# Kernel optimization log

Measured on AMD Instinct MI355X. Metric: run time of the kernel, lower is better.

The kernel has to match this reference:

```python
import jax, jax.numpy as jnp
import numpy as np
from jax.ops import segment_sum

N = 50000
E = 1600000
B = 1000  # number of graphs
F_IN, H, OUT = 64, 128, 10


def setup_inputs() -> dict:
    key = jax.random.key(0)
    ks = jax.random.split(key, 16)
    x = jax.random.normal(ks[0], (N, F_IN), dtype=jnp.float32)
    edge_index = jax.random.randint(ks[1], (2, E), 0, N, dtype=jnp.int64)
    batch = jnp.sort(jax.random.randint(ks[2], (N,), 0, B, dtype=jnp.int64))

    def glorot(k, fan_in, fan_out):
        s = jnp.sqrt(6.0 / (fan_in + fan_out))
        return jax.random.uniform(k, (fan_in, fan_out), jnp.float32, -s, s)

    return {
        "x": x, "edge_index": edge_index, "batch": batch,
        "W1": glorot(ks[3], F_IN, H), "b1": jnp.zeros((H,), jnp.float32),
        "W2": glorot(ks[4], H, H), "b2": jnp.zeros((H,), jnp.float32),
        "W3": glorot(ks[5], H, H // 2), "b3": jnp.zeros((H // 2,), jnp.float32),
        "Wl1": glorot(ks[6], H // 2, H // 4), "bl1": jnp.zeros((H // 4,), jnp.float32),
        "Wl2": glorot(ks[7], H // 4, OUT), "bl2": jnp.zeros((OUT,), jnp.float32),
    }


def _gcn_conv(x, src, dst, dinv, W, b):
    # GCNConv: h = x W; out_i = sum_{j->i} dinv_j * dinv_i * h_j ; + bias
    h = x @ W
    norm = dinv[src] * dinv[dst]                      # [E+N]
    msg = h[src] * norm[:, None]                      # gather + scale
    out = segment_sum(msg, dst, num_segments=N)       # scatter-add
    return out + b


def reference(x, edge_index, batch, W1, b1, W2, b2, W3, b3, Wl1, bl1, Wl2, bl2):
    # add self-loops (static shape E+N)
    loops = jnp.arange(N, dtype=edge_index.dtype)
    src = jnp.concatenate([edge_index[0], loops])
    dst = jnp.concatenate([edge_index[1], loops])
    # symmetric degree normalization from target degrees (incl. self-loops)
    deg = segment_sum(jnp.ones_like(dst, dtype=x.dtype), dst, num_segments=N)
    dinv = jnp.where(deg > 0, jax.lax.rsqrt(jnp.maximum(deg, 1.0)), 0.0)

    h = jax.nn.relu(_gcn_conv(x, src, dst, dinv, W1, b1))   # dropout: eval mode (identity)
    h = jax.nn.relu(_gcn_conv(h, src, dst, dinv, W2, b2))
    h = jax.nn.relu(_gcn_conv(h, src, dst, dinv, W3, b3))

    # global mean pool over graphs
    sums = segment_sum(h, batch, num_segments=B)            # [B, H//2]
    cnts = segment_sum(jnp.ones((N,), h.dtype), batch, num_segments=B)
    g = sums / jnp.maximum(cnts, 1.0)[:, None]

    g = jax.nn.relu(g @ Wl1 + bl1)
    return g @ Wl2 + bl2
```

## Files before the change

kernel.cpp:

```cpp
#include <hip/hip_runtime.h>
#include <hip/hip_bf16.h>
#include <hip/hip_fp16.h>

#define CHUNK 8192
#define WN    128
#define NBMAX 512

typedef _Float16 f16x8 __attribute__((ext_vector_type(8)));
typedef float    f32x4 __attribute__((ext_vector_type(4)));


__global__ __launch_bounds__(1024) void k_rhist(const int* __restrict__ dst, int* __restrict__ H,
                                                int E, int NC, int NB) {
    __shared__ int h[NBMAX];
    int c = blockIdx.x, t = threadIdx.x;
    for (int i = t; i < NB; i += 1024) h[i] = 0;
    __syncthreads();
    int base = c * CHUNK;
    int lim = min(CHUNK, E - base);
    for (int k = t; k < lim; k += 1024) atomicAdd(&h[dst[base + k] >> 7], 1);
    __syncthreads();
    for (int i = t; i < NB; i += 1024) H[i * NC + c] = h[i];
}

__global__ __launch_bounds__(256) void k_scanA(const int* __restrict__ in, int* __restrict__ out,
                                               int* __restrict__ bsum, int n) {
    __shared__ int s[256];
    int i = blockIdx.x * 256 + threadIdx.x;
    int v = (i < n) ? in[i] : 0;
    s[threadIdx.x] = v;
    __syncthreads();
    for (int off = 1; off < 256; off <<= 1) {
        int x = (threadIdx.x >= off) ? s[threadIdx.x - off] : 0;
        __syncthreads();
        s[threadIdx.x] += x;
        __syncthreads();
    }
    if (i < n) out[i] = s[threadIdx.x] - v;
    if (threadIdx.x == 255) bsum[blockIdx.x] = s[255];
}

__global__ __launch_bounds__(512) void k_scanB(int* __restrict__ bsum, int nb) {
    __shared__ int s[512];
    int t = threadIdx.x;
    int v = (t < nb) ? bsum[t] : 0;
    s[t] = v;
    __syncthreads();
    for (int off = 1; off < 512; off <<= 1) {
        int x = (t >= off) ? s[t - off] : 0;
        __syncthreads();
        s[t] += x;
        __syncthreads();
    }
    if (t < nb) bsum[t] = s[t] - v;
}

__global__ __launch_bounds__(256) void k_scanC(int* __restrict__ out, const int* __restrict__ bsum,
                                               int n) {
    int i = blockIdx.x * 256 + threadIdx.x;
    if (i < n) out[i] += bsum[blockIdx.x];
}

__global__ __launch_bounds__(1024) void k_rscatter(const int* __restrict__ src, const int* __restrict__ dst,
                                                   const int* __restrict__ O, int* __restrict__ packed,
                                                   int E, int NC, int NB) {
    __shared__ int cur[NBMAX];
    int c = blockIdx.x, t = threadIdx.x;
    for (int i = t; i < NB; i += 1024) cur[i] = O[i * NC + c];
    __syncthreads();
    int base = c * CHUNK;
    int lim = min(CHUNK, E - base);
    for (int k = t; k < lim; k += 1024) {
        int d = dst[base + k];
        int p = atomicAdd(&cur[d >> 7], 1);
        packed[p] = (src[base + k] << 7) | (d & (WN - 1));
    }
}

__global__ __launch_bounds__(512) void k_wincsr(const int* __restrict__ packed,
                                                const int* __restrict__ O,
                                                int* __restrict__ row_start,
                                                int* __restrict__ csr,
                                                float* __restrict__ dinv,
                                                const float* __restrict__ x,
                                                __half* __restrict__ y,
                                                int n, int NC, int NB, int E) {
    __shared__ int cnt[WN];
    __shared__ int ss[WN];
    __shared__ int cur[WN];
    __shared__ float sdv[WN];
    int b = blockIdx.x, t = threadIdx.x;
    int s = O[b * NC];
    int e = (b + 1 < NB) ? O[(b + 1) * NC] : E;
    if (t < WN) cnt[t] = 0;
    __syncthreads();
    for (int k = s + t; k < e; k += 512) atomicAdd(&cnt[packed[k] & (WN - 1)], 1);
    __syncthreads();
    int v = (t < WN) ? cnt[t] : 0;
    if (t < WN) ss[t] = v;
    __syncthreads();
    for (int off = 1; off < WN; off <<= 1) {
        int x2 = (t >= off && t < WN) ? ss[t - off] : 0;
        __syncthreads();
        if (t < WN) ss[t] += x2;
        __syncthreads();
    }
    int node = b * WN + t;
    if (t < WN) {
        int start = s + ss[t] - v;
        cur[t] = start;
        float dv = rsqrtf((float)(cnt[t] + 1));
        sdv[t] = dv;
        if (node < n) {
            row_start[node] = start;
            dinv[node] = dv;
        }
    }
    if (b == NB - 1 && t == 0) row_start[n] = E;
    __syncthreads();
    for (int k = s + t; k < e; k += 512) {
        int r = packed[k];
        int p = atomicAdd(&cur[r & (WN - 1)], 1);
        csr[p] = r >> 7;
    }
    int node0 = b * WN;
    for (int i = t; i < WN * 16; i += 512) {
        int nd = i >> 4, c4 = i & 15;
        int g = node0 + nd;
        if (g < n) {
            float dv = sdv[nd];
            float4 vv = ((const float4*)x)[(size_t)g * 16 + c4];
            __half2 h0 = __floats2half2_rn(vv.x * dv, vv.y * dv);
            __half2 h1 = __floats2half2_rn(vv.z * dv, vv.w * dv);
            uint2 u;
            u.x = *(unsigned int*)&h0;
            u.y = *(unsigned int*)&h1;
            ((uint2*)y)[(size_t)g * 16 + c4] = u;
        }
    }
}


__global__ __launch_bounds__(256) void k_w2h3(const float* __restrict__ W1, _Float16* __restrict__ W1t,
                                              const float* __restrict__ W2, _Float16* __restrict__ W2t,
                                              const float* __restrict__ W3, _Float16* __restrict__ W3t) {
    int idx = blockIdx.x * 256 + threadIdx.x;
    if (idx < 8192) {
        int k = idx >> 7, f = idx & 127;
        W1t[f * 64 + k] = (_Float16)W1[idx];
    } else if (idx < 24576) {
        int i = idx - 8192;
        int k = i >> 7, f = i & 127;
        W2t[f * 128 + k] = (_Float16)W2[i];
    } else if (idx < 32768) {
        int i = idx - 24576;
        int k = i >> 6, f = i & 63;
        W3t[f * 128 + k] = (_Float16)W3[i];
    }
}


template <int K, int F, int EPI, bool SP>
__global__ __launch_bounds__(256) void k_gemm_mfma(const __half* __restrict__ X,
                                                   const _Float16* __restrict__ Wt,
                                                   const float* __restrict__ dinv,
                                                   const float* __restrict__ bias,
                                                   __half* __restrict__ Hl,
                                                   __half* __restrict__ Hh, int n) {
    constexpr int ROWS = 64;
    constexpr int XS   = K + 8;
    __shared__ _Float16 sX[ROWS * XS];
    __shared__ _Float16 sW[F * XS];
    int row0 = blockIdx.x * ROWS;
    int t = threadIdx.x;

    const uint4* Xg = (const uint4*)X;
    for (int i = t; i < ROWS * (K / 8); i += 256) {
        int r = i / (K / 8), k8 = i % (K / 8);
        int gr = row0 + r;
        uint4 v = (gr < n) ? Xg[(size_t)gr * (K / 8) + k8] : make_uint4(0, 0, 0, 0);
        *(uint4*)&sX[r * XS + k8 * 8] = v;
    }
    const uint4* Wg = (const uint4*)Wt;
    for (int i = t; i < F * (K / 8); i += 256) {
        int f = i / (K / 8), k8 = i % (K / 8);
        *(uint4*)&sW[f * XS + k8 * 8] = Wg[i];
    }
    __syncthreads();

    int w = t >> 6, l = t & 63;
    int wrow = w * 16;
    int lr = l & 15;
    int lk = (l >> 4) * 8;
    f32x4 acc[F / 16];
#pragma unroll
    for (int c = 0; c < F / 16; ++c) acc[c] = (f32x4){0.f, 0.f, 0.f, 0.f};

#pragma unroll
    for (int kb = 0; kb < K / 32; ++kb) {
        f16x8 a = *(const f16x8*)&sX[(wrow + lr) * XS + kb * 32 + lk];
#pragma unroll
        for (int c = 0; c < F / 16; ++c) {
            f16x8 b = *(const f16x8*)&sW[(c * 16 + lr) * XS + kb * 32 + lk];
            acc[c] = __builtin_amdgcn_mfma_f32_16x16x32_f16(a, b, acc[c], 0, 0, 0);
        }
    }

    int rbase = row0 + wrow + (l >> 4) * 4;
    if (EPI == 0) {
        float dv[4];
#pragma unroll
        for (int r = 0; r < 4; ++r) dv[r] = (rbase + r < n) ? dinv[rbase + r] : 0.f;
#pragma unroll
        for (int c = 0; c < F / 16; ++c) {
            int col = c * 16 + lr;
#pragma unroll
            for (int r = 0; r < 4; ++r) {
                int gr = rbase + r;
                if (gr < n) {
                    __half hv = __float2half(acc[c][r] * dv[r]);
                    if (SP) {
                        if (c < F / 32) Hl[(size_t)gr * (F / 2) + col] = hv;
                        else            Hh[(size_t)gr * (F / 2) + col - F / 2] = hv;
                    } else {
                        Hl[(size_t)gr * F + col] = hv;
                    }
                }
            }
        }
    } else {
#pragma unroll
        for (int c = 0; c < F / 16; ++c) {
            int col = c * 16 + lr;
            float bc = bias[col];
#pragma unroll
            for (int r = 0; r < 4; ++r) {
                int gr = rbase + r;
                if (gr < n) {
                    __half hv = __float2half(fmaxf(acc[c][r] + bc, 0.f));
                    if (SP) {
                        if (c < F / 32) Hl[(size_t)gr * (F / 2) + col] = hv;
                        else            Hh[(size_t)gr * (F / 2) + col - F / 2] = hv;
                    } else {
                        Hl[(size_t)gr * F + col] = hv;
                    }
                }
            }
        }
    }
}


__device__ __forceinline__ void acc8(float* a, uint4 v) {
    const __half2* h = (const __half2*)&v;
#pragma unroll
    for (int i = 0; i < 4; ++i) {
        float2 f = __half22float2(h[i]);
        a[2 * i]     += f.x;
        a[2 * i + 1] += f.y;
    }
}

template <int F, int EPI>
__global__ void k_agg_h(const __half* __restrict__ HN, const int* __restrict__ csr,
                        const int* __restrict__ rs, const float* __restrict__ dinv,
                        const float* __restrict__ bias, __half* __restrict__ OUT,
                        int n, int ostride4, int ooff4) {
    constexpr int LPN = F / 8;
    constexpr int NPB = 256 / LPN;
    int node = blockIdx.x * NPB + threadIdx.x / LPN;
    int l    = threadIdx.x % LPN;
    if (node >= n) return;
    const uint4* hn = (const uint4*)HN;
    size_t base = (size_t)node * LPN + l;
    float a[8];
    {
        uint4 v = hn[base];
        const __half2* h = (const __half2*)&v;
#pragma unroll
        for (int i = 0; i < 4; ++i) {
            float2 f = __half22float2(h[i]);
            a[2 * i] = f.x; a[2 * i + 1] = f.y;
        }
    }
    int s = rs[node], e = rs[node + 1];
    int k = s;
    for (; k + 8 <= e; k += 8) {
        int si[8];
#pragma unroll
        for (int u = 0; u < 8; ++u) si[u] = csr[k + u];
        uint4 v[8];
#pragma unroll
        for (int u = 0; u < 8; ++u) v[u] = hn[(size_t)si[u] * LPN + l];
#pragma unroll
        for (int u = 0; u < 8; ++u) acc8(a, v[u]);
    }
    for (; k + 4 <= e; k += 4) {
        int s0 = csr[k], s1 = csr[k + 1], s2 = csr[k + 2], s3 = csr[k + 3];
        uint4 v0 = hn[(size_t)s0 * LPN + l];
        uint4 v1 = hn[(size_t)s1 * LPN + l];
        uint4 v2 = hn[(size_t)s2 * LPN + l];
        uint4 v3 = hn[(size_t)s3 * LPN + l];
        acc8(a, v0); acc8(a, v1); acc8(a, v2); acc8(a, v3);
    }
    for (; k < e; ++k) acc8(a, hn[(size_t)csr[k] * LPN + l]);

    float dv = dinv[node];
    float o[8];
    if (EPI == 0) {
#pragma unroll
        for (int j = 0; j < 8; ++j) o[j] = a[j] * dv;
    } else {
        const float4* b4 = (const float4*)bias;
        float4 bb0 = b4[l * 2], bb1 = b4[l * 2 + 1];
        o[0] = fmaxf(fmaf(a[0], dv, bb0.x), 0.f);
        o[1] = fmaxf(fmaf(a[1], dv, bb0.y), 0.f);
        o[2] = fmaxf(fmaf(a[2], dv, bb0.z), 0.f);
        o[3] = fmaxf(fmaf(a[3], dv, bb0.w), 0.f);
        o[4] = fmaxf(fmaf(a[4], dv, bb1.x), 0.f);
        o[5] = fmaxf(fmaf(a[5], dv, bb1.y), 0.f);
        o[6] = fmaxf(fmaf(a[6], dv, bb1.z), 0.f);
        o[7] = fmaxf(fmaf(a[7], dv, bb1.w), 0.f);
    }
    uint4 u;
    __half2 p0 = __floats2half2_rn(o[0], o[1]);
    __half2 p1 = __floats2half2_rn(o[2], o[3]);
    __half2 p2 = __floats2half2_rn(o[4], o[5]);
    __half2 p3 = __floats2half2_rn(o[6], o[7]);
    u.x = *(unsigned int*)&p0; u.y = *(unsigned int*)&p1;
    u.z = *(unsigned int*)&p2; u.w = *(unsigned int*)&p3;
    ((uint4*)OUT)[(size_t)node * ostride4 + ooff4 + l] = u;
}


__global__ void k_gstart(const int* __restrict__ batch, int* __restrict__ gstart,
                         int n, int B) {
    int i = blockIdx.x * 256 + threadIdx.x;
    if (i >= n) return;
    int b = batch[i];
    if (i == 0) {
        for (int g = 0; g <= b; ++g) gstart[g] = 0;
    } else {
        int prev = batch[i - 1];
        if (prev != b)
            for (int g = prev + 1; g <= b; ++g) gstart[g] = i;
    }
    if (i == n - 1)
        for (int g = b + 1; g <= B; ++g) gstart[g] = n;
}

__global__ void k_poolhead(const __half* __restrict__ H3, const int* __restrict__ gstart,
                           const float* __restrict__ Wl1, const float* __restrict__ bl1,
                           const float* __restrict__ Wl2, const float* __restrict__ bl2,
                           float* __restrict__ out, int B) {
    __shared__ float sh[4][64];
    __shared__ float shid[4][32];
    int w = threadIdx.x >> 6;
    int lane = threadIdx.x & 63;
    int g = blockIdx.x * 4 + w;
    if (g < B) {
        int s = gstart[g], e = gstart[g + 1];
        float acc = 0.f;
        for (int i = s; i < e; ++i) acc += __half2float(H3[(size_t)i * 64 + lane]);
        float cnt = fmaxf((float)(e - s), 1.f);
        sh[w][lane] = acc / cnt;
    }
    __syncthreads();
    if (g < B && lane < 32) {
        float a = bl1[lane];
        for (int k = 0; k < 64; ++k) a = fmaf(sh[w][k], Wl1[k * 32 + lane], a);
        shid[w][lane] = fmaxf(a, 0.f);
    }
    __syncthreads();
    if (g < B && lane < 10) {
        float a = bl2[lane];
        for (int k = 0; k < 32; ++k) a = fmaf(shid[w][k], Wl2[k * 10 + lane], a);
        out[g * 10 + lane] = a;
    }
}


extern "C" void kernel_launch(void* const* d_in, const int* in_sizes, int n_in,
                              void* d_out, int out_size, void* d_ws, size_t ws_size,
                              hipStream_t stream) {
    const float* x    = (const float*)d_in[0];
    const int*   ei   = (const int*)d_in[1];
    const int*   batch= (const int*)d_in[2];
    const float* W1   = (const float*)d_in[3];
    const float* b1   = (const float*)d_in[4];
    const float* W2   = (const float*)d_in[5];
    const float* b2   = (const float*)d_in[6];
    const float* W3   = (const float*)d_in[7];
    const float* b3   = (const float*)d_in[8];
    const float* Wl1  = (const float*)d_in[9];
    const float* bl1  = (const float*)d_in[10];
    const float* Wl2  = (const float*)d_in[11];
    const float* bl2  = (const float*)d_in[12];

    const int N  = in_sizes[0] / 64;
    const int E  = in_sizes[1] / 2;
    const int B  = out_size / 10;
    const int NB = (N + WN - 1) / WN;
    const int NC = (E + CHUNK - 1) / CHUNK;
    const int NBNC = NB * NC;
    const int GS = (NBNC + 255) / 256;
    const int* srcI = ei;
    const int* dstI = ei + E;

    char* p = (char*)d_ws;
    auto alloc = [&](size_t bytes) {
        char* r = p;
        p += (bytes + 255) & ~(size_t)255;
        return r;
    };
    int*   H        = (int*)alloc((size_t)NBNC * 4);
    int*   O        = (int*)alloc((size_t)NBNC * 4);
    int*   bsum     = (int*)alloc(2048 * 4);
    int*   packed   = (int*)alloc((size_t)E * 4);
    int*   csr      = (int*)alloc((size_t)E * 4);
    int*   row_start= (int*)alloc((size_t)(N + 1) * 4);
    float* dinv     = (float*)alloc((size_t)N * 4);
    int*   gstart   = (int*)alloc((size_t)(B + 1) * 4);
    _Float16* W1t   = (_Float16*)alloc((size_t)64 * 128 * 2);
    _Float16* W2t   = (_Float16*)alloc((size_t)128 * 128 * 2);
    _Float16* W3t   = (_Float16*)alloc((size_t)128 * 64 * 2);
    __half* bufA    = (__half*)alloc((size_t)N * 128 * 2);
    __half* bufB    = (__half*)alloc((size_t)N * 128 * 2);
    __half* bufB2   = bufB + (size_t)N * 64;

    int gN = (N + 255) / 256;
    int gG = (N + 63) / 64;

    k_rhist   <<<NC, 1024, 0, stream>>>(dstI, H, E, NC, NB);
    k_scanA   <<<GS, 256, 0, stream>>>(H, O, bsum, NBNC);
    k_scanB   <<<1, 512, 0, stream>>>(bsum, GS);
    k_scanC   <<<GS, 256, 0, stream>>>(O, bsum, NBNC);
    k_rscatter<<<NC, 1024, 0, stream>>>(srcI, dstI, O, packed, E, NC, NB);
    k_wincsr  <<<NB, 512, 0, stream>>>(packed, O, row_start, csr, dinv, x, bufA,
                                       N, NC, NB, E);

    k_w2h3<<<128, 256, 0, stream>>>(W1, W1t, W2, W2t, W3, W3t);

    k_agg_h<64, 0><<<(N + 31) / 32, 256, 0, stream>>>(bufA, csr, row_start, dinv,
                                                      dinv, bufB, N, 8, 0);
    k_gemm_mfma<64, 128, 1, false><<<gG, 256, 0, stream>>>(bufB, W1t, dinv, b1,
                                                           bufA, nullptr, N);
    k_gemm_mfma<128, 128, 0, true><<<gG, 256, 0, stream>>>(bufA, W2t, dinv, b2,
                                                           bufB, bufB2, N);
    k_agg_h<64, 1><<<(N + 31) / 32, 256, 0, stream>>>(bufB,  csr, row_start, dinv,
                                                      b2,      bufA, N, 16, 0);
    k_agg_h<64, 1><<<(N + 31) / 32, 256, 0, stream>>>(bufB2, csr, row_start, dinv,
                                                      b2 + 64, bufA, N, 16, 8);
    k_gemm_mfma<128, 64, 0, false><<<gG, 256, 0, stream>>>(bufA, W3t, dinv, b3,
                                                           bufB, nullptr, N);
    k_agg_h<64, 1><<<(N + 31) / 32, 256, 0, stream>>>(bufB, csr, row_start, dinv,
                                                      b3, bufB2, N, 8, 0);

    k_gstart  <<<gN, 256, 0, stream>>>(batch, gstart, N, B);
    k_poolhead<<<(B + 3) / 4, 256, 0, stream>>>(bufB2, gstart, Wl1, bl1, Wl2, bl2,
                                                (float*)d_out, B);
}
```

Baseline: 205.2 us.

## Fuse scan fixup, merge layer-2 aggregations, fold mean-pool into last aggregation

Drops the scanC kernel by adding the block prefix offsets directly where O is read in the scatter and window-CSR kernels. The two per-half aggregation launches of layer 2 become a single launch that uses a 2-D grid. The final aggregation no longer writes H3; it atomically adds each node's output into per-graph float sums and counts, which removes the gstart kernel and the serial per-graph sum loop in the pool head. In exchange there are many float atomics on 1000 graph rows, a memset of the accumulators, and a summation order that is no longer deterministic.

```diff
diff --git a/kernel.cpp b/kernel.cpp
--- a/kernel.cpp
+++ b/kernel.cpp
@@ -55,18 +55,16 @@
     if (t < nb) bsum[t] = s[t] - v;
 }
 
-__global__ __launch_bounds__(256) void k_scanC(int* __restrict__ out, const int* __restrict__ bsum,
-                                               int n) {
-    int i = blockIdx.x * 256 + threadIdx.x;
-    if (i < n) out[i] += bsum[blockIdx.x];
-}
 
 __global__ __launch_bounds__(1024) void k_rscatter(const int* __restrict__ src, const int* __restrict__ dst,
-                                                   const int* __restrict__ O, int* __restrict__ packed,
-                                                   int E, int NC, int NB) {
+                                                   const int* __restrict__ O, const int* __restrict__ bsum,
+                                                   int* __restrict__ packed, int E, int NC, int NB) {
     __shared__ int cur[NBMAX];
     int c = blockIdx.x, t = threadIdx.x;
-    for (int i = t; i < NB; i += 1024) cur[i] = O[i * NC + c];
+    for (int i = t; i < NB; i += 1024) {
+        int idx = i * NC + c;
+        cur[i] = O[idx] + bsum[idx >> 8];
+    }
     __syncthreads();
     int base = c * CHUNK;
     int lim = min(CHUNK, E - base);
@@ -79,6 +77,7 @@
 
 __global__ __launch_bounds__(512) void k_wincsr(const int* __restrict__ packed,
                                                 const int* __restrict__ O,
+                                                const int* __restrict__ bsum,
                                                 int* __restrict__ row_start,
                                                 int* __restrict__ csr,
                                                 float* __restrict__ dinv,
@@ -90,8 +89,15 @@
     __shared__ int cur[WN];
     __shared__ float sdv[WN];
     int b = blockIdx.x, t = threadIdx.x;
-    int s = O[b * NC];
-    int e = (b + 1 < NB) ? O[(b + 1) * NC] : E;
+    int i0 = b * NC;
+    int s = O[i0] + bsum[i0 >> 8];
+    int e;
+    if (b + 1 < NB) {
+        int i1 = (b + 1) * NC;
+        e = O[i1] + bsum[i1 >> 8];
+    } else {
+        e = E;
+    }
     if (t < WN) cnt[t] = 0;
     __syncthreads();
     for (int k = s + t; k < e; k += 512) atomicAdd(&cnt[packed[k] & (WN - 1)], 1);
@@ -261,13 +267,20 @@
     }
 }
 
-template <int F, int EPI>
-__global__ void k_agg_h(const __half* __restrict__ HN, const int* __restrict__ csr,
-                        const int* __restrict__ rs, const float* __restrict__ dinv,
-                        const float* __restrict__ bias, __half* __restrict__ OUT,
-                        int n, int ostride4, int ooff4) {
+template <int F, int EPI, int POOL>
+__global__ void k_agg_h(const __half* __restrict__ HN0, const __half* __restrict__ HN1,
+                        const int* __restrict__ csr, const int* __restrict__ rs,
+                        const float* __restrict__ dinv,
+                        const float* __restrict__ bias0, const float* __restrict__ bias1,
+                        __half* __restrict__ OUT, int n, int ostride4,
+                        const int* __restrict__ batch, float* __restrict__ gsum,
+                        int* __restrict__ gcnt) {
     constexpr int LPN = F / 8;
     constexpr int NPB = 256 / LPN;
+    int half = blockIdx.y;
+    const __half* HN = half ? HN1 : HN0;
+    const float* bias = half ? bias1 : bias0;
+    int ooff4 = half ? LPN : 0;
     int node = blockIdx.x * NPB + threadIdx.x / LPN;
     int l    = threadIdx.x % LPN;
     if (node >= n) return;
@@ -322,34 +335,26 @@
         o[6] = fmaxf(fmaf(a[6], dv, bb1.z), 0.f);
         o[7] = fmaxf(fmaf(a[7], dv, bb1.w), 0.f);
     }
-    uint4 u;
-    __half2 p0 = __floats2half2_rn(o[0], o[1]);
-    __half2 p1 = __floats2half2_rn(o[2], o[3]);
-    __half2 p2 = __floats2half2_rn(o[4], o[5]);
-    __half2 p3 = __floats2half2_rn(o[6], o[7]);
-    u.x = *(unsigned int*)&p0; u.y = *(unsigned int*)&p1;
-    u.z = *(unsigned int*)&p2; u.w = *(unsigned int*)&p3;
-    ((uint4*)OUT)[(size_t)node * ostride4 + ooff4 + l] = u;
-}
-
-
-__global__ void k_gstart(const int* __restrict__ batch, int* __restrict__ gstart,
-                         int n, int B) {
-    int i = blockIdx.x * 256 + threadIdx.x;
-    if (i >= n) return;
-    int b = batch[i];
-    if (i == 0) {
-        for (int g = 0; g <= b; ++g) gstart[g] = 0;
+    if (POOL) {
+        int bg = batch[node];
+        float* gs = &gsum[bg * 64 + l * 8];
+#pragma unroll
+        for (int j = 0; j < 8; ++j) atomicAdd(&gs[j], o[j]);
+        if (l == 0) atomicAdd(&gcnt[bg], 1);
     } else {
-        int prev = batch[i - 1];
-        if (prev != b)
-            for (int g = prev + 1; g <= b; ++g) gstart[g] = i;
-    }
-    if (i == n - 1)
-        for (int g = b + 1; g <= B; ++g) gstart[g] = n;
-}
-
-__global__ void k_poolhead(const __half* __restrict__ H3, const int* __restrict__ gstart,
+        uint4 u;
+        __half2 p0 = __floats2half2_rn(o[0], o[1]);
+        __half2 p1 = __floats2half2_rn(o[2], o[3]);
+        __half2 p2 = __floats2half2_rn(o[4], o[5]);
+        __half2 p3 = __floats2half2_rn(o[6], o[7]);
+        u.x = *(unsigned int*)&p0; u.y = *(unsigned int*)&p1;
+        u.z = *(unsigned int*)&p2; u.w = *(unsigned int*)&p3;
+        ((uint4*)OUT)[(size_t)node * ostride4 + ooff4 + l] = u;
+    }
+}
+
+
+__global__ void k_poolhead(const float* __restrict__ gsum, const int* __restrict__ gcnt,
                            const float* __restrict__ Wl1, const float* __restrict__ bl1,
                            const float* __restrict__ Wl2, const float* __restrict__ bl2,
                            float* __restrict__ out, int B) {
@@ -359,11 +364,8 @@
     int lane = threadIdx.x & 63;
     int g = blockIdx.x * 4 + w;
     if (g < B) {
-        int s = gstart[g], e = gstart[g + 1];
-        float acc = 0.f;
-        for (int i = s; i < e; ++i) acc += __half2float(H3[(size_t)i * 64 + lane]);
-        float cnt = fmaxf((float)(e - s), 1.f);
-        sh[w][lane] = acc / cnt;
+        float cnt = fmaxf((float)gcnt[g], 1.f);
+        sh[w][lane] = gsum[g * 64 + lane] / cnt;
     }
     __syncthreads();
     if (g < B && lane < 32) {
@@ -413,6 +415,9 @@
         p += (bytes + 255) & ~(size_t)255;
         return r;
     };
+    float* gsum     = (float*)alloc((size_t)B * 64 * 4);
+    int*   gcnt     = (int*)alloc((size_t)B * 4);
+    size_t zbytes   = (size_t)(p - (char*)d_ws);
     int*   H        = (int*)alloc((size_t)NBNC * 4);
     int*   O        = (int*)alloc((size_t)NBNC * 4);
     int*   bsum     = (int*)alloc(2048 * 4);
@@ -420,7 +425,6 @@
     int*   csr      = (int*)alloc((size_t)E * 4);
     int*   row_start= (int*)alloc((size_t)(N + 1) * 4);
     float* dinv     = (float*)alloc((size_t)N * 4);
-    int*   gstart   = (int*)alloc((size_t)(B + 1) * 4);
     _Float16* W1t   = (_Float16*)alloc((size_t)64 * 128 * 2);
     _Float16* W2t   = (_Float16*)alloc((size_t)128 * 128 * 2);
     _Float16* W3t   = (_Float16*)alloc((size_t)128 * 64 * 2);
@@ -428,35 +432,36 @@
     __half* bufB    = (__half*)alloc((size_t)N * 128 * 2);
     __half* bufB2   = bufB + (size_t)N * 64;
 
-    int gN = (N + 255) / 256;
     int gG = (N + 63) / 64;
+    int gA = (N + 31) / 32;
+
+    hipMemsetAsync(d_ws, 0, zbytes, stream);
 
     k_rhist   <<<NC, 1024, 0, stream>>>(dstI, H, E, NC, NB);
     k_scanA   <<<GS, 256, 0, stream>>>(H, O, bsum, NBNC);
     k_scanB   <<<1, 512, 0, stream>>>(bsum, GS);
-    k_scanC   <<<GS, 256, 0, stream>>>(O, bsum, NBNC);
-    k_rscatter<<<NC, 1024, 0, stream>>>(srcI, dstI, O, packed, E, NC, NB);
-    k_wincsr  <<<NB, 512, 0, stream>>>(packed, O, row_start, csr, dinv, x, bufA,
+    k_rscatter<<<NC, 1024, 0, stream>>>(srcI, dstI, O, bsum, packed, E, NC, NB);
+    k_wincsr  <<<NB, 512, 0, stream>>>(packed, O, bsum, row_start, csr, dinv, x, bufA,
                                        N, NC, NB, E);
 
     k_w2h3<<<128, 256, 0, stream>>>(W1, W1t, W2, W2t, W3, W3t);
 
-    k_agg_h<64, 0><<<(N + 31) / 32, 256, 0, stream>>>(bufA, csr, row_start, dinv,
-                                                      dinv, bufB, N, 8, 0);
+    k_agg_h<64, 0, 0><<<dim3(gA, 1), 256, 0, stream>>>(bufA, bufA, csr, row_start, dinv,
+                                                       dinv, dinv, bufB, N, 8,
+                                                       batch, gsum, gcnt);
     k_gemm_mfma<64, 128, 1, false><<<gG, 256, 0, stream>>>(bufB, W1t, dinv, b1,
                                                            bufA, nullptr, N);
     k_gemm_mfma<128, 128, 0, true><<<gG, 256, 0, stream>>>(bufA, W2t, dinv, b2,
                                                            bufB, bufB2, N);
-    k_agg_h<64, 1><<<(N + 31) / 32, 256, 0, stream>>>(bufB,  csr, row_start, dinv,
-                                                      b2,      bufA, N, 16, 0);
-    k_agg_h<64, 1><<<(N + 31) / 32, 256, 0, stream>>>(bufB2, csr, row_start, dinv,
-                                                      b2 + 64, bufA, N, 16, 8);
+    k_agg_h<64, 1, 0><<<dim3(gA, 2), 256, 0, stream>>>(bufB, bufB2, csr, row_start, dinv,
+                                                       b2, b2 + 64, bufA, N, 16,
+                                                       batch, gsum, gcnt);
     k_gemm_mfma<128, 64, 0, false><<<gG, 256, 0, stream>>>(bufA, W3t, dinv, b3,
                                                            bufB, nullptr, N);
-    k_agg_h<64, 1><<<(N + 31) / 32, 256, 0, stream>>>(bufB, csr, row_start, dinv,
-                                                      b3, bufB2, N, 8, 0);
-
-    k_gstart  <<<gN, 256, 0, stream>>>(batch, gstart, N, B);
-    k_poolhead<<<(B + 3) / 4, 256, 0, stream>>>(bufB2, gstart, Wl1, bl1, Wl2, bl2,
+    k_agg_h<64, 1, 1><<<dim3(gA, 1), 256, 0, stream>>>(bufB, bufB, csr, row_start, dinv,
+                                                       b3, b3, nullptr, N, 0,
+                                                       batch, gsum, gcnt);
+
+    k_poolhead<<<(B + 3) / 4, 256, 0, stream>>>(gsum, gcnt, Wl1, bl1, Wl2, bl2,
                                                 (float*)d_out, B);
 }
```

Result: slower. 322.1 us (+57.0%).
